# Kernel optimization log

Hardware: AMD Instinct MI355X
Metric: run time of the kernel (lower is better)

Reference implementation:

```python
import jax, jax.numpy as jnp
import numpy as np

K = 2  # kernel_size


def setup_inputs() -> dict:
    key = jax.random.key(0)
    k1, k2, k3, k4, k5 = jax.random.split(key, 5)
    B, C, H, W_sp = 8, 256, 128, 128
    N = 512                      # number of keypoints
    E = C * K * K                # embed_dim = 1024
    img_feat_highres = jax.random.normal(k1, (B, C, H, W_sp), dtype=jnp.float32)
    W = jax.random.normal(k2, (E, C, K, K), dtype=jnp.float32) * 0.02  # conv weight, OIHW
    b = jax.random.normal(k3, (E,), dtype=jnp.float32) * 0.02          # conv bias
    batch_indices = jnp.broadcast_to(jnp.arange(B, dtype=jnp.int64)[:, None], (B, N))
    pixel_x_id = jax.random.randint(k4, (B, N), 0, H // 2, dtype=jnp.int64)  # low-res ids
    pixel_y_id = jax.random.randint(k5, (B, N), 0, H // 2, dtype=jnp.int64)
    return {
        "img_feat_highres": img_feat_highres,
        "W": W,
        "b": b,
        "batch_indices": batch_indices,
        "pixel_x_id": pixel_x_id,
        "pixel_y_id": pixel_y_id,
    }


def reference(img_feat_highres, W, b, batch_indices, pixel_x_id, pixel_y_id):
    # Dense conv2d, stride 1, padding = K-1 (torch nn.Conv2d semantics)
    patches = jax.lax.conv_general_dilated(
        img_feat_highres, W,
        window_strides=(1, 1),
        padding=((K - 1, K - 1), (K - 1, K - 1)),
        dimension_numbers=("NCHW", "OIHW", "NCHW"),
    ) + b[None, :, None, None]  # (B, E, H+K-1, W+K-1)

    y0 = 2 * pixel_y_id  # (B, N)
    x0 = 2 * pixel_x_id

    def samp(dy, dx):
        # advanced indices at dims 0,2,3 (non-adjacent) -> result (B, N, E)
        return patches[batch_indices, :, y0 + dy, x0 + dx]

    local_feat = jnp.concatenate(
        [samp(0, 0), samp(K, 0), samp(0, K), samp(K, K)], axis=2
    )  # (B, N, 4E)
    return jnp.transpose(local_feat, (0, 2, 1))  # (B, 4E, N)
```

## Files before the change

kernel.cpp:

```cpp
#include <hip/hip_runtime.h>
#include <stdint.h>


typedef __attribute__((ext_vector_type(8))) short bf16x8;
typedef __attribute__((ext_vector_type(4))) float f32x4;

#define GAS(p) ((const __attribute__((address_space(1))) void*)(p))
#define LAS(p) ((__attribute__((address_space(3))) void*)(p))

__device__ __forceinline__ unsigned short f2bf(float f) {
    union { float f; uint32_t u; } x; x.f = f;
    uint32_t u = x.u;
    uint32_t r = (u + 0x7FFFu + ((u >> 16) & 1u)) >> 16;
    return (unsigned short)r;
}

__global__ __launch_bounds__(256)
void prep_kernel(const float* __restrict__ img, const float* __restrict__ Wf,
                 unsigned short* __restrict__ Wq, unsigned short* __restrict__ zp,
                 unsigned short* __restrict__ imgT) {
    __shared__ unsigned short sT[8192];
    const int blk = blockIdx.x;
    const int tid = threadIdx.x;

    if (blk < 512) {
        if (blk == 0 && tid < 32) {
            uint4 z = {0, 0, 0, 0};
            ((uint4*)zp)[tid] = z;
        }
        const int t  = blk * 256 + tid;
        const int et = t >> 15;
        const int r1 = t & 32767;
        const int jt = r1 >> 10;
        const int r2 = r1 & 1023;
        const int chunk = r2 >> 8;
        const int row   = r2 & 255;
        const int e  = et * 256 + row;
        const int kb = jt * 32 + chunk * 8;
        unsigned short v[8];
        #pragma unroll
        for (int kk = 0; kk < 8; ++kk) {
            const int k = kb + kk;
            const int c = k & 255;
            const int p = k >> 8;
            v[kk] = f2bf(Wf[(size_t)e * 1024 + c * 4 + p]);
        }
        *(uint4*)&Wq[(size_t)t * 8] = *(const uint4*)v;
        return;
    }

    const int ib = blk - 512;
    const int cc = ib & 3;
    const int y  = (ib >> 2) & 127;
    const int b  = ib >> 9;
    const int xq = tid & 31;
    const int ch = tid >> 5;
    unsigned int* sU = (unsigned int*)sT;
    const size_t pl = ((size_t)b * 256 + cc * 64) * 16384 + (size_t)y * 128;
    #pragma unroll
    for (int it = 0; it < 4; ++it) {
        const int cp = it * 8 + ch;
        const float4 v0 = *(const float4*)&img[pl + (size_t)(2 * cp)     * 16384 + xq * 4];
        const float4 v1 = *(const float4*)&img[pl + (size_t)(2 * cp + 1) * 16384 + xq * 4];
        const float a0[4] = {v0.x, v0.y, v0.z, v0.w};
        const float a1[4] = {v1.x, v1.y, v1.z, v1.w};
        #pragma unroll
        for (int jj = 0; jj < 4; ++jj) {
            const int x = xq * 4 + jj;
            const unsigned int pk = (unsigned)f2bf(a0[jj]) | ((unsigned)f2bf(a1[jj]) << 16);
            sU[x * 32 + (cp ^ (x & 31))] = pk;
        }
    }
    __syncthreads();
    unsigned short* ob = imgT + (((size_t)b * 128 + y) * 128) * 256 + cc * 64;
    #pragma unroll
    for (int jj = 0; jj < 16; ++jj) {
        const int oo = tid + 256 * jj;
        const int xx = oo >> 5;
        const int c2 = oo & 31;
        const unsigned int pk = sU[xx * 32 + (c2 ^ (xx & 31))];
        *(unsigned int*)&ob[(size_t)xx * 256 + c2 * 2] = pk;
    }
}

__global__ __launch_bounds__(512, 1)
void gemm_kernel(const unsigned short* __restrict__ Wq,
                 const unsigned short* __restrict__ imgT,
                 const unsigned short* __restrict__ zp,
                 const int* __restrict__ bidx,
                 const int* __restrict__ pxid,
                 const int* __restrict__ pyid,
                 const float* __restrict__ bias,
                 float* __restrict__ out)
{
    const int orig = blockIdx.x;
    const int xcd  = orig & 7;
    const int s    = orig >> 3;
    const int gnt  = xcd * 8 + (s >> 2);
    const int et   = s & 3;
    const int e0   = et * 256;
    const int g    = gnt >> 1;
    const int n0   = (gnt & 1) * 256;
    const int b = g >> 2, o = g & 3;

    const int tid  = threadIdx.x;
    const int lane = tid & 63;
    const int wid  = tid >> 6;
    const int wm   = wid >> 2;
    const int wn   = wid & 3;

    __shared__ unsigned short sW[4][8192];
    __shared__ unsigned short sA[4][8192];

    int ayv[2], axv[2];
    size_t apl[2];
    #pragma unroll
    for (int u = 0; u < 2; ++u) {
        const int row = u * 128 + (tid >> 2);
        const int gi = b * 512 + n0 + row;
        apl[u] = (size_t)bidx[gi] * (128 * 128 * 256);
        ayv[u] = 2 * pyid[gi] - 1 + (o & 1) * 2;
        axv[u] = 2 * pxid[gi] - 1 + (o >> 1) * 2;
    }
    const int aswz = (((tid & 3) ^ ((tid >> 3) & 3))) * 8;
    const unsigned short* wq_base = Wq + (size_t)et * 262144 + tid * 8;

    f32x4 acc[8][4];
    #pragma unroll
    for (int m = 0; m < 8; ++m)
        #pragma unroll
        for (int nf = 0; nf < 4; ++nf) acc[m][nf] = (f32x4){0.f, 0.f, 0.f, 0.f};

    auto stage = [&](int jt, int buf) {
        #pragma unroll
        for (int u = 0; u < 2; ++u)
            __builtin_amdgcn_global_load_lds(GAS(wq_base + (size_t)jt * 8192 + u * 4096),
                LAS(&sW[buf][u * 4096 + tid * 8]), 16, 0, 0);
        const int p   = jt >> 3;
        const int csh = (jt & 7) * 32 + aswz;
        #pragma unroll
        for (int u = 0; u < 2; ++u) {
            const int yy = ayv[u] + (p >> 1);
            const int xx = axv[u] + (p & 1);
            const unsigned short* src =
                ((unsigned)yy < 128u && (unsigned)xx < 128u)
                    ? imgT + apl[u] + ((size_t)(yy * 128 + xx)) * 256 + csh
                    : zp + aswz;
            __builtin_amdgcn_global_load_lds(GAS(src),
                LAS(&sA[buf][u * 4096 + tid * 8]), 16, 0, 0);
        }
    };

    stage(0, 0);
    stage(1, 1);
    stage(2, 2);

    for (int j = 0; j < 32; ++j) {
        const int buf = j & 3;
        if (j < 30)      { asm volatile("s_waitcnt vmcnt(8)" ::: "memory"); }
        else if (j == 30){ asm volatile("s_waitcnt vmcnt(4)" ::: "memory"); }
        else             { asm volatile("s_waitcnt vmcnt(0)" ::: "memory"); }
        __builtin_amdgcn_s_barrier();
        if (j + 3 < 32) stage(j + 3, (j + 3) & 3);

        bf16x8 af[8];
        {
            const int chunk = lane >> 4;
            const int rb = wm * 128 + (lane & 15);
            #pragma unroll
            for (int m = 0; m < 8; ++m)
                af[m] = *(const bf16x8*)&sW[buf][chunk * 2048 + (rb + m * 16) * 8];
        }
        #pragma unroll
        for (int nh = 0; nh < 2; ++nh) {
            bf16x8 bfr[2];
            #pragma unroll
            for (int nn = 0; nn < 2; ++nn) {
                const int row = wn * 64 + (nh * 2 + nn) * 16 + (lane & 15);
                const int perm = (lane >> 4) ^ ((row >> 1) & 3);
                bfr[nn] = *(const bf16x8*)&sA[buf][row * 32 + perm * 8];
            }
            __builtin_amdgcn_s_setprio(1);
            #pragma unroll
            for (int m = 0; m < 8; ++m)
                #pragma unroll
                for (int nn = 0; nn < 2; ++nn)
                    acc[m][nh * 2 + nn] = __builtin_amdgcn_mfma_f32_16x16x32_bf16(
                        af[m], bfr[nn], acc[m][nh * 2 + nn], 0, 0, 0);
            __builtin_amdgcn_s_setprio(0);
        }
    }

    #pragma unroll
    for (int m = 0; m < 8; ++m) {
        const int eb = e0 + wm * 128 + m * 16 + (lane >> 4) * 4;
        float bv[4];
        #pragma unroll
        for (int reg = 0; reg < 4; ++reg) bv[reg] = bias[eb + reg];
        #pragma unroll
        for (int nf = 0; nf < 4; ++nf) {
            const int nn = n0 + wn * 64 + nf * 16 + (lane & 15);
            #pragma unroll
            for (int reg = 0; reg < 4; ++reg)
                out[((size_t)g * 1024 + eb + reg) * 512 + nn] = acc[m][nf][reg] + bv[reg];
        }
    }
}

extern "C" void kernel_launch(void* const* d_in, const int* in_sizes, int n_in,
                              void* d_out, int out_size, void* d_ws, size_t ws_size,
                              hipStream_t stream) {
    const float* img  = (const float*)d_in[0];
    const float* Wf   = (const float*)d_in[1];
    const float* bias = (const float*)d_in[2];
    const int*   bidx = (const int*)d_in[3];
    const int*   pxid = (const int*)d_in[4];
    const int*   pyid = (const int*)d_in[5];
    float* out = (float*)d_out;

    unsigned short* Wq   = (unsigned short*)((char*)d_ws + (32u << 20));
    unsigned short* zp   = (unsigned short*)((char*)d_ws + (36u << 20));
    unsigned short* imgT = (unsigned short*)((char*)d_ws + (64u << 20));

    hipLaunchKernelGGL(prep_kernel, dim3(4608), dim3(256), 0, stream,
                       img, Wf, Wq, zp, imgT);
    hipLaunchKernelGGL(gemm_kernel, dim3(256), dim3(512), 0, stream,
                       Wq, imgT, zp, bidx, pxid, pyid, bias, out);
}
```

Baseline: 87.38 us.

## Retile gather-GEMM to full-E blocks with 64 keypoints and split W/A pipelines

Each block now computes all 1024 output channels for 64 keypoints instead of 256x256 tiles, so each gathered image row is loaded once per block rather than re-gathered by four E-tiles. Weights are re-laid out in prep as 32-wide K tiles over the full E range and streamed through a double-buffered LDS ring, while the A operand uses a separate triple-buffered ring refilled every two steps. This removes redundant gather traffic but makes every block stream the whole weight matrix, increases LDS use, and adds a second barrier per iteration.

```diff
diff --git a/kernel.cpp b/kernel.cpp
--- a/kernel.cpp
+++ b/kernel.cpp
@@ -28,15 +28,12 @@
             uint4 z = {0, 0, 0, 0};
             ((uint4*)zp)[tid] = z;
         }
-        const int t  = blk * 256 + tid;
-        const int et = t >> 15;
-        const int r1 = t & 32767;
-        const int jt = r1 >> 10;
-        const int r2 = r1 & 1023;
-        const int chunk = r2 >> 8;
-        const int row   = r2 & 255;
-        const int e  = et * 256 + row;
-        const int kb = jt * 32 + chunk * 8;
+        const int t    = blk * 256 + tid;
+        const int tile = t >> 12;
+        const int r    = t & 4095;
+        const int kc   = r >> 10;
+        const int e    = r & 1023;
+        const int kb   = tile * 32 + kc * 8;
         unsigned short v[8];
         #pragma unroll
         for (int kk = 0; kk < 8; ++kk) {
@@ -93,37 +90,42 @@
                  const float* __restrict__ bias,
                  float* __restrict__ out)
 {
-    const int orig = blockIdx.x;
-    const int xcd  = orig & 7;
-    const int s    = orig >> 3;
-    const int gnt  = xcd * 8 + (s >> 2);
-    const int et   = s & 3;
-    const int e0   = et * 256;
-    const int g    = gnt >> 1;
-    const int n0   = (gnt & 1) * 256;
+    const int tile = blockIdx.x;
+    const int g    = tile >> 3;
+    const int n0   = (tile & 7) * 64;
     const int b = g >> 2, o = g & 3;
 
     const int tid  = threadIdx.x;
     const int lane = tid & 63;
-    const int wid  = tid >> 6;
-    const int wm   = wid >> 2;
-    const int wn   = wid & 3;
-
-    __shared__ unsigned short sW[4][8192];
-    __shared__ unsigned short sA[4][8192];
-
-    int ayv[2], axv[2];
-    size_t apl[2];
-    #pragma unroll
-    for (int u = 0; u < 2; ++u) {
-        const int row = u * 128 + (tid >> 2);
-        const int gi = b * 512 + n0 + row;
-        apl[u] = (size_t)bidx[gi] * (128 * 128 * 256);
-        ayv[u] = 2 * pyid[gi] - 1 + (o & 1) * 2;
-        axv[u] = 2 * pxid[gi] - 1 + (o >> 1) * 2;
-    }
-    const int aswz = (((tid & 3) ^ ((tid >> 3) & 3))) * 8;
-    const unsigned short* wq_base = Wq + (size_t)et * 262144 + tid * 8;
+    const int w    = tid >> 6;
+
+    __shared__ unsigned short sW[2][32768];
+    __shared__ unsigned short sA[3][4096];
+
+    const int arow = tid >> 3;
+    const int sg   = (tid & 7) ^ (arow & 7);
+    const int gi   = b * 512 + n0 + arow;
+    const size_t apl = (size_t)bidx[gi] * (128 * 128 * 256);
+    const int ay0 = 2 * pyid[gi] - 1 + (o & 1) * 2;
+    const int ax0 = 2 * pxid[gi] - 1 + (o >> 1) * 2;
+
+    auto stageA = [&](int pp, int abuf) {
+        const int p  = pp >> 2;
+        const int yy = ay0 + (p >> 1);
+        const int xx = ax0 + (p & 1);
+        const unsigned short* src =
+            ((unsigned)yy < 128u && (unsigned)xx < 128u)
+                ? imgT + apl + ((size_t)(yy * 128 + xx)) * 256 + (pp & 3) * 64 + sg * 8
+                : zp + sg * 8;
+        __builtin_amdgcn_global_load_lds(GAS(src), LAS(&sA[abuf][tid * 8]), 16, 0, 0);
+    };
+    auto stageW = [&](int j, int wbuf) {
+        const unsigned short* base = Wq + (size_t)j * 32768 + tid * 8;
+        #pragma unroll
+        for (int u = 0; u < 8; ++u)
+            __builtin_amdgcn_global_load_lds(GAS(base + u * 4096),
+                LAS(&sW[wbuf][u * 4096 + tid * 8]), 16, 0, 0);
+    };
 
     f32x4 acc[8][4];
     #pragma unroll
@@ -131,75 +133,55 @@
         #pragma unroll
         for (int nf = 0; nf < 4; ++nf) acc[m][nf] = (f32x4){0.f, 0.f, 0.f, 0.f};
 
-    auto stage = [&](int jt, int buf) {
-        #pragma unroll
-        for (int u = 0; u < 2; ++u)
-            __builtin_amdgcn_global_load_lds(GAS(wq_base + (size_t)jt * 8192 + u * 4096),
-                LAS(&sW[buf][u * 4096 + tid * 8]), 16, 0, 0);
-        const int p   = jt >> 3;
-        const int csh = (jt & 7) * 32 + aswz;
-        #pragma unroll
-        for (int u = 0; u < 2; ++u) {
-            const int yy = ayv[u] + (p >> 1);
-            const int xx = axv[u] + (p & 1);
-            const unsigned short* src =
-                ((unsigned)yy < 128u && (unsigned)xx < 128u)
-                    ? imgT + apl[u] + ((size_t)(yy * 128 + xx)) * 256 + csh
-                    : zp + aswz;
-            __builtin_amdgcn_global_load_lds(GAS(src),
-                LAS(&sA[buf][u * 4096 + tid * 8]), 16, 0, 0);
-        }
-    };
-
-    stage(0, 0);
-    stage(1, 1);
-    stage(2, 2);
-
+    stageA(0, 0); stageA(1, 1); stageW(0, 0); stageW(1, 1);
+
+    int prd = 0;
+    int pst = 2;
+    #pragma unroll 2
     for (int j = 0; j < 32; ++j) {
-        const int buf = j & 3;
-        if (j < 30)      { asm volatile("s_waitcnt vmcnt(8)" ::: "memory"); }
-        else if (j == 30){ asm volatile("s_waitcnt vmcnt(4)" ::: "memory"); }
-        else             { asm volatile("s_waitcnt vmcnt(0)" ::: "memory"); }
+        if (j == 31)    { asm volatile("s_waitcnt vmcnt(0)" ::: "memory"); }
+        else if (j & 1) { asm volatile("s_waitcnt vmcnt(9)" ::: "memory"); }
+        else            { asm volatile("s_waitcnt vmcnt(8)" ::: "memory"); }
         __builtin_amdgcn_s_barrier();
-        if (j + 3 < 32) stage(j + 3, (j + 3) & 3);
-
+        if (!(j & 1) && j <= 26) {
+            stageA((j >> 1) + 2, pst);
+            pst = (pst == 2) ? 0 : pst + 1;
+        }
+
+        const int wbuf = j & 1;
+        const int kc = lane >> 4;
         bf16x8 af[8];
-        {
-            const int chunk = lane >> 4;
-            const int rb = wm * 128 + (lane & 15);
-            #pragma unroll
-            for (int m = 0; m < 8; ++m)
-                af[m] = *(const bf16x8*)&sW[buf][chunk * 2048 + (rb + m * 16) * 8];
-        }
-        #pragma unroll
-        for (int nh = 0; nh < 2; ++nh) {
-            bf16x8 bfr[2];
-            #pragma unroll
-            for (int nn = 0; nn < 2; ++nn) {
-                const int row = wn * 64 + (nh * 2 + nn) * 16 + (lane & 15);
-                const int perm = (lane >> 4) ^ ((row >> 1) & 3);
-                bfr[nn] = *(const bf16x8*)&sA[buf][row * 32 + perm * 8];
-            }
+        #pragma unroll
+        for (int m = 0; m < 8; ++m) {
+            const int e = w * 128 + m * 16 + (lane & 15);
+            af[m] = *(const bf16x8*)&sW[wbuf][(kc * 1024 + e) * 8];
+        }
+        #pragma unroll
+        for (int nf = 0; nf < 4; ++nf) {
+            const int row = nf * 16 + (lane & 15);
+            const int sl  = (wbuf * 4 + kc) ^ (row & 7);
+            const bf16x8 bfr = *(const bf16x8*)&sA[prd][(row * 8 + sl) * 8];
             __builtin_amdgcn_s_setprio(1);
             #pragma unroll
             for (int m = 0; m < 8; ++m)
-                #pragma unroll
-                for (int nn = 0; nn < 2; ++nn)
-                    acc[m][nh * 2 + nn] = __builtin_amdgcn_mfma_f32_16x16x32_bf16(
-                        af[m], bfr[nn], acc[m][nh * 2 + nn], 0, 0, 0);
+                acc[m][nf] = __builtin_amdgcn_mfma_f32_16x16x32_bf16(
+                    af[m], bfr, acc[m][nf], 0, 0, 0);
             __builtin_amdgcn_s_setprio(0);
         }
+        __builtin_amdgcn_s_barrier();
+        if (j & 1) prd = (prd == 2) ? 0 : prd + 1;
+        if (j <= 29) stageW(j + 2, wbuf);
     }
 
     #pragma unroll
     for (int m = 0; m < 8; ++m) {
-        const int eb = e0 + wm * 128 + m * 16 + (lane >> 4) * 4;
+        const int eb = w * 128 + m * 16 + (lane >> 4) * 4;
         float bv[4];
         #pragma unroll
         for (int reg = 0; reg < 4; ++reg) bv[reg] = bias[eb + reg];
         #pragma unroll
         for (int nf = 0; nf < 4; ++nf) {
-            const int nn = n0 + wn * 64 + nf * 16 + (lane & 15);
+            const int nn = n0 + nf * 16 + (lane & 15);
             #pragma unroll
             for (int reg = 0; reg < 4; ++reg)
                 out[((size_t)g * 1024 + eb + reg) * 512 + nn] = acc[m][nf][reg] + bv[reg];
```

Result: slower. 92.41 us (+5.8%).
